# Performance work log

Measured on AMD Instinct MI355X. Metric: run time of the kernel, lower is better.

The kernel has to match this reference:

```python
import jax, jax.numpy as jnp
import numpy as np

EPS = 1e-6
NEG_SLOPE = 0.01  # torch LeakyReLU default

def ln(x, g, b):
    m = jnp.mean(x, axis=-1, keepdims=True)
    v = jnp.mean((x - m) ** 2, axis=-1, keepdims=True)
    return (x - m) / jnp.sqrt(v + EPS) * g + b

def leaky(x):
    return jnp.where(x >= 0, x, NEG_SLOPE * x)

def setup_inputs() -> dict:
    B, L, F, H, NH, LBL = 8, 1024, 1024, 256, 8, 4766
    key = jax.random.key(0)
    ks = jax.random.split(key, 16)
    def lin(k, i, o, s=0.03):
        kw, kb = jax.random.split(k)
        return jax.random.normal(kw, (i, o), jnp.float32) * s, jnp.zeros((o,), jnp.float32)
    w_in, b_in = lin(ks[0], F, H)
    w_h, b_h = lin(ks[1], H, H)
    a_w1, a_b1 = lin(ks[2], H, 64)
    a_w2, a_b2 = lin(ks[3], 64, NH)
    o_w1, o_b1 = lin(ks[4], NH * H, NH * H)
    o_w2, o_b2 = lin(ks[5], NH * H, LBL)
    CM = (jax.random.uniform(ks[6], (LBL, LBL)) < 0.002).astype(jnp.float32)
    CM = jnp.maximum(CM, jnp.eye(LBL, dtype=jnp.float32))
    return {
        'h_V': jax.random.normal(ks[7], (B, L, F), jnp.float32),
        'mask': jnp.ones((B, L), jnp.int32),
        'ln0_g': jnp.ones((F,), jnp.float32), 'ln0_b': jnp.zeros((F,), jnp.float32),
        'w_in': w_in, 'b_in': b_in,
        'ln1_g': jnp.ones((H,), jnp.float32), 'ln1_b': jnp.zeros((H,), jnp.float32),
        'w_h': w_h, 'b_h': b_h,
        'ln2_g': jnp.ones((H,), jnp.float32), 'ln2_b': jnp.zeros((H,), jnp.float32),
        'a_w1': a_w1, 'a_b1': a_b1,
        'a_lng': jnp.ones((64,), jnp.float32), 'a_lnb': jnp.zeros((64,), jnp.float32),
        'a_w2': a_w2, 'a_b2': a_b2,
        'o_w1': o_w1, 'o_b1': o_b1,
        'o_lng': jnp.ones((NH * H,), jnp.float32), 'o_lnb': jnp.zeros((NH * H,), jnp.float32),
        'o_w2': o_w2, 'o_b2': o_b2,
        'CM': CM,
    }

def reference(h_V, mask, ln0_g, ln0_b, w_in, b_in, ln1_g, ln1_b, w_h, b_h,
              ln2_g, ln2_b, a_w1, a_b1, a_lng, a_lnb, a_w2, a_b2,
              o_w1, o_b1, o_lng, o_lnb, o_w2, o_b2, CM):
    B = h_V.shape[0]
    # input + hidden blocks (eval mode: dropout is identity)
    x = ln(h_V, ln0_g, ln0_b)
    x = leaky(x @ w_in + b_in)
    x = ln(x, ln1_g, ln1_b)
    x = leaky(x @ w_h + b_h)
    x = ln(x, ln2_g, ln2_b)                      # [B,L,H]
    # multi-head attention pooling over sequence
    a = leaky(x @ a_w1 + a_b1)
    a = ln(a, a_lng, a_lnb)
    a = a @ a_w2 + a_b2                          # [B,L,NH]
    a = jnp.where(mask[:, :, None] == 0, jnp.float32(-1e9), a)
    a = jax.nn.softmax(a, axis=1)
    h = jnp.einsum('blh,bld->bhd', a, x).reshape(B, -1)  # [B,NH*H]
    # output block
    h = leaky(h @ o_w1 + o_b1)
    h = ln(h, o_lng, o_lnb)
    p = jax.nn.sigmoid(h @ o_w2 + o_b2)          # [B,LBL]
    # GO-hierarchy max-product propagation (eval path)
    out = jnp.max(p[:, None, :] * CM[None, :, :], axis=-1)  # [B,LBL]
    return out.astype(jnp.float32)
```

## Files before the change

### kernel.cpp

```cpp
#include <hip/hip_runtime.h>
#include <hip/hip_bf16.h>
#include <cstdint>

#define B_   8
#define L_   1024
#define F_   1024
#define H_   256
#define NH_  8
#define LBL_ 4766
#define M_   (B_*L_)
#define OD_  (NH_*H_)
#define NCM  (LBL_*LBL_)
#define MP_EPB 16384
#define MP_NB  ((NCM + MP_EPB - 1) / MP_EPB)

typedef unsigned short u16;
typedef unsigned int   u32;
typedef __attribute__((ext_vector_type(8))) short short8;
typedef __attribute__((ext_vector_type(4))) float float4v;

#define BF16_ONES_PAIR 0x3f803f80u

__device__ __forceinline__ float bf2f(u32 u) { return __uint_as_float(u << 16); }
__device__ __forceinline__ u16 f2bf(float f) {
    u32 u = __float_as_uint(f);
    u32 r = 0x7fffu + ((u >> 16) & 1u);
    return (u16)((u + r) >> 16);
}

struct f8 { float v[8]; };

__device__ __forceinline__ float ldS(const void* p, size_t i, bool bf) {
    return bf ? bf2f(((const u16*)p)[i]) : ((const float*)p)[i];
}
__device__ __forceinline__ float4 ld4(const void* p, size_t i, bool bf) {
    if (bf) {
        uint2 u = *(const uint2*)((const u16*)p + i);
        return make_float4(bf2f(u.x & 0xffff), bf2f(u.x >> 16),
                           bf2f(u.y & 0xffff), bf2f(u.y >> 16));
    }
    return *(const float4*)((const float*)p + i);
}
__device__ __forceinline__ f8 ld8(const void* p, size_t i, bool bf) {
    f8 r;
    if (bf) {
        uint4 u = *(const uint4*)((const u16*)p + i);
        r.v[0]=bf2f(u.x&0xffff); r.v[1]=bf2f(u.x>>16);
        r.v[2]=bf2f(u.y&0xffff); r.v[3]=bf2f(u.y>>16);
        r.v[4]=bf2f(u.z&0xffff); r.v[5]=bf2f(u.z>>16);
        r.v[6]=bf2f(u.w&0xffff); r.v[7]=bf2f(u.w>>16);
    } else {
        const float* q = (const float*)p + i;
        float4 a = *(const float4*)q, b = *(const float4*)(q+4);
        r.v[0]=a.x; r.v[1]=a.y; r.v[2]=a.z; r.v[3]=a.w;
        r.v[4]=b.x; r.v[5]=b.y; r.v[6]=b.z; r.v[7]=b.w;
    }
    return r;
}

__device__ __forceinline__ float wave_sum(float v) {
    #pragma unroll
    for (int m = 1; m < 64; m <<= 1) v += __shfl_xor(v, m, 64);
    return v;
}
__device__ __forceinline__ float wave_max(float v) {
    #pragma unroll
    for (int m = 1; m < 64; m <<= 1) v = fmaxf(v, __shfl_xor(v, m, 64));
    return v;
}
__device__ __forceinline__ float blk_sum(float v, float* sh) {
    v = wave_sum(v);
    int w = threadIdx.x >> 6, nw = blockDim.x >> 6;
    if ((threadIdx.x & 63) == 0) sh[w] = v;
    __syncthreads();
    float s = sh[0];
    for (int i = 1; i < nw; ++i) s += sh[i];
    __syncthreads();
    return s;
}
__device__ __forceinline__ float blk_max(float v, float* sh) {
    v = wave_max(v);
    int w = threadIdx.x >> 6, nw = blockDim.x >> 6;
    if ((threadIdx.x & 63) == 0) sh[w] = v;
    __syncthreads();
    float s = sh[0];
    for (int i = 1; i < nw; ++i) s = fmaxf(s, sh[i]);
    __syncthreads();
    return s;
}

__global__ __launch_bounds__(256) void prep_k(const void* __restrict__ hv,
        const void* __restrict__ g0, const void* __restrict__ b0, u16* __restrict__ x0,
        const void* __restrict__ w_in, u16* __restrict__ wt1,
        const void* __restrict__ w_h,  u16* __restrict__ wt2,
        const void* __restrict__ aw1,  u16* __restrict__ wt3,
        float* __restrict__ zA, float* __restrict__ zB,
        const u32* __restrict__ probe) {
    __shared__ u16 tile[64][65];
    bool bf = (probe[0] == BF16_ONES_PAIR);
    int blk = blockIdx.x, t = threadIdx.x;
    if (blk < M_/4) {
        int row = (blk << 2) + (t >> 6);
        int l = t & 63;
        size_t base = (size_t)row * F_;
        float4 vv[4];
        float s = 0.f, q = 0.f;
        #pragma unroll
        for (int j = 0; j < 4; ++j) {
            float4 v = ld4(hv, base + l * 4 + j * 256, bf);
            vv[j] = v;
            s += v.x + v.y + v.z + v.w;
            q += v.x*v.x + v.y*v.y + v.z*v.z + v.w*v.w;
        }
        s = wave_sum(s);
        q = wave_sum(q);
        float mean = s * (1.f / F_);
        float rstd = rsqrtf(q * (1.f / F_) - mean * mean + 1e-6f);
        #pragma unroll
        for (int j = 0; j < 4; ++j) {
            int off = l * 4 + j * 256;
            float4 gg = ld4(g0, off, bf);
            float4 bb = ld4(b0, off, bf);
            float4 v = vv[j];
            u32 o0 = f2bf((v.x - mean) * rstd * gg.x + bb.x)
                   | ((u32)f2bf((v.y - mean) * rstd * gg.y + bb.y) << 16);
            u32 o1 = f2bf((v.z - mean) * rstd * gg.z + bb.z)
                   | ((u32)f2bf((v.w - mean) * rstd * gg.w + bb.w) << 16);
            *(uint2*)(x0 + base + off) = make_uint2(o0, o1);
        }
        return;
    }
    blk -= M_/4;
    const void* W = nullptr; u16* WT = nullptr; int K = 0, N = 0, kt = 0, nt = 0;
    if (blk < 64)      { W = w_in; WT = wt1; K = F_; N = H_; kt = blk & 15; nt = blk >> 4; }
    else if (blk < 80) { int j = blk - 64; W = w_h; WT = wt2; K = H_; N = H_; kt = j & 3; nt = j >> 2; }
    else if (blk < 84) { int j = blk - 80; W = aw1; WT = wt3; K = H_; N = 64; kt = j; nt = 0; }
    else {
        int j = blk - 84;
        if (j < 16) {
            float4* p = (float4*)zA;
            for (int i = j * 256 + t; i < 8192; i += 4096) p[i] = make_float4(0,0,0,0);
        } else {
            j -= 16;
            float4* p = (float4*)zB;
            for (int i = j * 256 + t; i < 13628; i += 4096) p[i] = make_float4(0,0,0,0);
        }
        return;
    }
    int kt0 = kt * 64, nt0 = nt * 64;
    int r = t >> 2, cq = (t & 3) * 16;
    #pragma unroll
    for (int j = 0; j < 4; ++j) {
        float4 v = ld4(W, (size_t)(kt0 + r) * N + nt0 + cq + j * 4, bf);
        tile[r][cq + j*4 + 0] = f2bf(v.x);
        tile[r][cq + j*4 + 1] = f2bf(v.y);
        tile[r][cq + j*4 + 2] = f2bf(v.z);
        tile[r][cq + j*4 + 3] = f2bf(v.w);
    }
    __syncthreads();
    #pragma unroll
    for (int j = 0; j < 4; ++j) {
        int k = cq + j * 4;
        u32 a0 = tile[k+0][r], a1 = tile[k+1][r], a2 = tile[k+2][r], a3 = tile[k+3][r];
        uint2 o; o.x = a0 | (a1 << 16); o.y = a2 | (a3 << 16);
        *(uint2*)(WT + (size_t)(nt0 + r) * K + kt0 + k) = o;
    }
}

__global__ __launch_bounds__(256) void gemm_mfma(const u16* __restrict__ Ap, int amode,
        const float2* __restrict__ statin, const void* __restrict__ g,
        const void* __restrict__ bta, const u16* __restrict__ WT,
        const void* __restrict__ bias, u16* __restrict__ C,
        float* __restrict__ statout, int M, int N, int K,
        const u32* __restrict__ probe) {
    __shared__ short8 As[2][64][5];
    __shared__ short8 Bs[2][64][5];
    bool pbf = (probe[0] == BF16_ONES_PAIR);
    int t = threadIdx.x;
    int m0 = blockIdx.x * 64, n0 = blockIdx.y * 64;
    int r = t >> 2, kq = t & 3;
    int l = t & 63, w = t >> 6;
    int q = l >> 4, ml = l & 15;
    float4v acc[4];
    #pragma unroll
    for (int nt = 0; nt < 4; ++nt)
        #pragma unroll
        for (int i = 0; i < 4; ++i) acc[nt][i] = 0.f;
    float stm = 0.f, str = 1.f;
    if (amode == 1) {
        float2 st = statin[m0 + r];
        float mm = st.x * (1.f / K);
        stm = mm;
        str = rsqrtf(st.y * (1.f / K) - mm * mm + 1e-6f);
    }
    const size_t arow = (size_t)(m0 + r) * K;
    const size_t brow = (size_t)(n0 + r) * K;
    auto loadA = [&](int kk) -> short8 {
        if (amode == 1) {
            f8 a  = ld8(Ap, arow + kk, true);
            f8 gg = ld8(g, kk, pbf);
            f8 bb = ld8(bta, kk, pbf);
            short8 pa;
            #pragma unroll
            for (int j = 0; j < 8; ++j)
                pa[j] = (short)f2bf((a.v[j] - stm) * str * gg.v[j] + bb.v[j]);
            return pa;
        }
        return *(const short8*)(Ap + arow + kk);
    };
    {
        short8 pa = loadA(kq * 8);
        short8 pb = *(const short8*)(WT + brow + kq * 8);
        As[0][r][kq] = pa;
        Bs[0][r][kq] = pb;
    }
    __syncthreads();
    int nIt = K >> 5, cur = 0;
    for (int it = 0; it < nIt; ++it) {
        bool more = (it + 1 < nIt);
        short8 na, nb;
        if (more) {
            int kk = (it + 1) * 32 + kq * 8;
            na = loadA(kk);
            nb = *(const short8*)(WT + brow + kk);
        }
        short8 af = As[cur][w * 16 + ml][q];
        #pragma unroll
        for (int nt = 0; nt < 4; ++nt)
            acc[nt] = __builtin_amdgcn_mfma_f32_16x16x32_bf16(af, Bs[cur][nt*16 + ml][q],
                                                              acc[nt], 0, 0, 0);
        if (more) {
            As[cur ^ 1][r][kq] = na;
            Bs[cur ^ 1][r][kq] = nb;
            __syncthreads();
            cur ^= 1;
        }
    }
    float ov[4][4];
    #pragma unroll
    for (int nt = 0; nt < 4; ++nt) {
        int nn = n0 + nt * 16 + ml;
        float bv = ldS(bias, nn, pbf);
        #pragma unroll
        for (int reg = 0; reg < 4; ++reg) {
            float v = acc[nt][reg] + bv;
            v = v >= 0.f ? v : 0.01f * v;
            ov[nt][reg] = v;
            C[(size_t)(m0 + w * 16 + q * 4 + reg) * N + nn] = f2bf(v);
        }
    }
    if (statout) {
        #pragma unroll
        for (int reg = 0; reg < 4; ++reg) {
            float sv = ov[0][reg] + ov[1][reg] + ov[2][reg] + ov[3][reg];
            float qv = ov[0][reg]*ov[0][reg] + ov[1][reg]*ov[1][reg]
                     + ov[2][reg]*ov[2][reg] + ov[3][reg]*ov[3][reg];
            #pragma unroll
            for (int mk = 1; mk < 16; mk <<= 1) {
                sv += __shfl_xor(sv, mk, 64);
                qv += __shfl_xor(qv, mk, 64);
            }
            if (ml == 0) {
                int row = m0 + w * 16 + q * 4 + reg;
                atomicAdd(&statout[2 * row],     sv);
                atomicAdd(&statout[2 * row + 1], qv);
            }
        }
    }
}

__global__ __launch_bounds__(256) void gemm3_attn_k(const u16* __restrict__ Ap,
        const float2* __restrict__ statin, const void* __restrict__ g,
        const void* __restrict__ bta, const u16* __restrict__ WT,
        const void* __restrict__ bias,
        const void* __restrict__ alng, const void* __restrict__ alnb,
        const void* __restrict__ aw2, const void* __restrict__ ab2,
        const int* __restrict__ mask, float* __restrict__ lg,
        const u32* __restrict__ probe) {
    __shared__ short8 As[2][64][5];
    __shared__ short8 Bs[2][64][5];
    __shared__ float at[64][65];
    __shared__ float w2s[512];
    __shared__ float b2s[8];
    __shared__ float gs[64], bs[64];
    bool pbf = (probe[0] == BF16_ONES_PAIR);
    const int K = 256;
    int t = threadIdx.x;
    int m0 = blockIdx.x * 64;
    int r = t >> 2, kq = t & 3;
    int l = t & 63, w = t >> 6;
    int q = l >> 4, ml = l & 15;
    float4v acc[4];
    #pragma unroll
    for (int nt = 0; nt < 4; ++nt)
        #pragma unroll
        for (int i = 0; i < 4; ++i) acc[nt][i] = 0.f;
    float2 st = statin[m0 + r];
    float stm = st.x * (1.f / K);
    float str = rsqrtf(st.y * (1.f / K) - stm * stm + 1e-6f);
    const size_t arow = (size_t)(m0 + r) * K;
    const size_t brow = (size_t)r * K;
    auto loadA = [&](int kk) -> short8 {
        f8 a  = ld8(Ap, arow + kk, true);
        f8 gg = ld8(g, kk, pbf);
        f8 bb = ld8(bta, kk, pbf);
        short8 pa;
        #pragma unroll
        for (int j = 0; j < 8; ++j)
            pa[j] = (short)f2bf((a.v[j] - stm) * str * gg.v[j] + bb.v[j]);
        return pa;
    };
    {
        short8 pa = loadA(kq * 8);
        short8 pb = *(const short8*)(WT + brow + kq * 8);
        As[0][r][kq] = pa;
        Bs[0][r][kq] = pb;
    }
    __syncthreads();
    int cur = 0;
    #pragma unroll
    for (int it = 0; it < 8; ++it) {
        bool more = (it < 7);
        short8 na, nb;
        if (more) {
            int kk = (it + 1) * 32 + kq * 8;
            na = loadA(kk);
            nb = *(const short8*)(WT + brow + kk);
        }
        short8 af = As[cur][w * 16 + ml][q];
        #pragma unroll
        for (int nt = 0; nt < 4; ++nt)
            acc[nt] = __builtin_amdgcn_mfma_f32_16x16x32_bf16(af, Bs[cur][nt*16 + ml][q],
                                                              acc[nt], 0, 0, 0);
        if (more) {
            As[cur ^ 1][r][kq] = na;
            Bs[cur ^ 1][r][kq] = nb;
            __syncthreads();
            cur ^= 1;
        }
    }
    for (int i = t; i < 512; i += 256) w2s[i] = ldS(aw2, i, pbf);
    if (t < 8) b2s[t] = ldS(ab2, t, pbf);
    if (t < 64) { gs[t] = ldS(alng, t, pbf); bs[t] = ldS(alnb, t, pbf); }
    #pragma unroll
    for (int nt = 0; nt < 4; ++nt) {
        int nn = nt * 16 + ml;
        float bv = ldS(bias, nn, pbf);
        #pragma unroll
        for (int reg = 0; reg < 4; ++reg) {
            float v = acc[nt][reg] + bv;
            v = v >= 0.f ? v : 0.01f * v;
            at[w * 16 + q * 4 + reg][nn] = v;
        }
    }
    __syncthreads();
    int row = t >> 2, s4 = t & 3;
    float av[16];
    float sum = 0.f, sq = 0.f;
    #pragma unroll
    for (int j = 0; j < 16; ++j) {
        float v = at[row][s4 * 16 + j];
        av[j] = v; sum += v; sq += v * v;
    }
    sum += __shfl_xor(sum, 1, 64); sum += __shfl_xor(sum, 2, 64);
    sq  += __shfl_xor(sq, 1, 64);  sq  += __shfl_xor(sq, 2, 64);
    float mr = sum * (1.f / 64);
    float rr = rsqrtf(sq * (1.f / 64) - mr * mr + 1e-6f);
    float val[16];
    #pragma unroll
    for (int j = 0; j < 16; ++j)
        val[j] = (av[j] - mr) * rr * gs[s4 * 16 + j] + bs[s4 * 16 + j];
    float hv[8];
    #pragma unroll
    for (int h = 0; h < 8; ++h) {
        float p = 0.f;
        #pragma unroll
        for (int j = 0; j < 16; ++j) p += val[j] * w2s[(s4 * 16 + j) * 8 + h];
        p += __shfl_xor(p, 1, 64);
        p += __shfl_xor(p, 2, 64);
        hv[h] = p + b2s[h];
    }
    if (s4 == 0) {
        int gr = m0 + row;
        bool mz = (mask[gr] == 0);
        int bb_ = gr >> 10, ll = gr & 1023;
        #pragma unroll
        for (int h = 0; h < 8; ++h) {
            float v = mz ? -1e9f : hv[h];
            lg[((size_t)bb_ * NH_ + h) * L_ + ll] = v;
        }
    }
}

__global__ __launch_bounds__(1024) void attnpool_k(const float* __restrict__ lg,
        const float2* __restrict__ st2, const u16* __restrict__ x2,
        const void* __restrict__ g, const void* __restrict__ b,
        float* __restrict__ hp, const u32* __restrict__ probe) {
    __shared__ float aw_s[1024];
    __shared__ float part[16][256];
    __shared__ float sh[16];
    bool pbf = (probe[0] == BF16_ONES_PAIR);
    int bh = blockIdx.x, t = threadIdx.x;
    int bb = bh >> 3;
    float v = lg[(size_t)bh * L_ + t];
    float mx = blk_max(v, sh);
    float e = expf(v - mx);
    float s = blk_sum(e, sh);
    float inv = 1.f / s;
    float2 st = st2[(bb << 10) + t];
    float m = st.x * (1.f / 256);
    float r = rsqrtf(st.y * (1.f / 256) - m * m + 1e-6f);
    float aw = e * inv * r;
    aw_s[t] = aw;
    float c1 = blk_sum(aw * m, sh);
    int chunk = t >> 6, d0 = (t & 63) * 4;
    const u16* xb = x2 + ((size_t)(bb << 10) + chunk * 64) * 256;
    const float* awc = aw_s + chunk * 64;
    float a0 = 0.f, a1 = 0.f, a2 = 0.f, a3 = 0.f;
    #pragma unroll 8
    for (int i = 0; i < 64; ++i) {
        uint2 u = *(const uint2*)(xb + (size_t)i * 256 + d0);
        float wv = awc[i];
        a0 += wv * bf2f(u.x & 0xffff);
        a1 += wv * bf2f(u.x >> 16);
        a2 += wv * bf2f(u.y & 0xffff);
        a3 += wv * bf2f(u.y >> 16);
    }
    *(float4*)&part[chunk][d0] = make_float4(a0, a1, a2, a3);
    __syncthreads();
    if (t < 256) {
        float S = 0.f;
        #pragma unroll
        for (int c = 0; c < 16; ++c) S += part[c][t];
        hp[(size_t)bh * 256 + t] = (S - c1) * ldS(g, t, pbf) + ldS(b, t, pbf);
    }
}

template<int KC>
__global__ __launch_bounds__(256) void gemv_ilp_k(const float* __restrict__ hv,
        const void* __restrict__ W, float* __restrict__ acc, int K, int N,
        const u32* __restrict__ probe) {
    __shared__ float hs[8 * KC];
    bool bf = (probe[0] == BF16_ONES_PAIR);
    int t = threadIdx.x;
    int kb = blockIdx.y * KC;
    for (int i = t; i < 8 * KC; i += 256) {
        int r = i / KC, k = i & (KC - 1);
        hs[i] = hv[(size_t)r * K + kb + k];
    }
    __syncthreads();
    int c0 = (blockIdx.x * 256 + t) * 2;
    if (c0 >= N) return;
    float a[8][2] = {};
    if (bf) {
        const u16* Wp = (const u16*)W;
        #pragma unroll
        for (int h = 0; h < KC / 32; ++h) {
            u32 wr[32];
            #pragma unroll
            for (int i = 0; i < 32; ++i)
                wr[i] = *(const u32*)(Wp + (size_t)(kb + h * 32 + i) * N + c0);
            #pragma unroll
            for (int i = 0; i < 32; ++i) {
                float w0 = bf2f(wr[i] & 0xffff), w1 = bf2f(wr[i] >> 16);
                #pragma unroll
                for (int r = 0; r < 8; ++r) {
                    float hh = hs[r * KC + h * 32 + i];
                    a[r][0] += hh * w0; a[r][1] += hh * w1;
                }
            }
        }
    } else {
        const float* Wp = (const float*)W;
        #pragma unroll
        for (int h = 0; h < KC / 16; ++h) {
            float2 wr[16];
            #pragma unroll
            for (int i = 0; i < 16; ++i)
                wr[i] = *(const float2*)(Wp + (size_t)(kb + h * 16 + i) * N + c0);
            #pragma unroll
            for (int i = 0; i < 16; ++i) {
                #pragma unroll
                for (int r = 0; r < 8; ++r) {
                    float hh = hs[r * KC + h * 16 + i];
                    a[r][0] += hh * wr[i].x; a[r][1] += hh * wr[i].y;
                }
            }
        }
    }
    bool ok1 = (c0 + 1 < N);
    #pragma unroll
    for (int r = 0; r < 8; ++r) {
        atomicAdd(&acc[(size_t)r * N + c0], a[r][0]);
        if (ok1) atomicAdd(&acc[(size_t)r * N + c0 + 1], a[r][1]);
    }
}

__global__ __launch_bounds__(256) void out_ln_k(float* __restrict__ h,
        const void* __restrict__ bias, const void* __restrict__ g,
        const void* __restrict__ b, const u32* __restrict__ probe) {
    __shared__ float sh[4];
    bool bf = (probe[0] == BF16_ONES_PAIR);
    int row = blockIdx.x, t = threadIdx.x;
    float v[8];
    float s = 0.f, q = 0.f;
    #pragma unroll
    for (int i = 0; i < 8; ++i) {
        int c = t + i * 256;
        float x = h[(size_t)row * OD_ + c] + ldS(bias, c, bf);
        x = x >= 0.f ? x : 0.01f * x;
        v[i] = x; s += x; q += x * x;
    }
    s = blk_sum(s, sh) * (1.f / OD_);
    q = blk_sum(q, sh) * (1.f / OD_);
    float rstd = rsqrtf(q - s * s + 1e-6f);
    #pragma unroll
    for (int i = 0; i < 8; ++i) {
        int c = t + i * 256;
        h[(size_t)row * OD_ + c] = (v[i] - s) * rstd * ldS(g, c, bf) + ldS(b, c, bf);
    }
}

__global__ __launch_bounds__(256) void sigmoid_t_k(const float* __restrict__ acc,
        const void* __restrict__ bias, float* __restrict__ pt,
        float* __restrict__ out, const u32* __restrict__ probe) {
    bool bf = (probe[0] == BF16_ONES_PAIR);
    int c = blockIdx.x * 256 + threadIdx.x;
    if (c >= LBL_) return;
    float bv = ldS(bias, c, bf);
    float o[8];
    #pragma unroll
    for (int r = 0; r < 8; ++r) {
        float v = acc[(size_t)r * LBL_ + c] + bv;
        o[r] = 1.f / (1.f + expf(-v));
        out[(size_t)r * LBL_ + c] = 0.f;
    }
    float4* dst = (float4*)(pt + (size_t)c * 8);
    dst[0] = make_float4(o[0], o[1], o[2], o[3]);
    dst[1] = make_float4(o[4], o[5], o[6], o[7]);
}

__device__ __forceinline__ void mp_hit(u32 idx, float cmv,
        const float* __restrict__ pt, int* smax, u32 rowBase) {
    u32 i = idx / LBL_;
    u32 j = idx - i * LBL_;
    const float4* pj = (const float4*)(pt + (size_t)j * 8);
    float4 pa = pj[0], pb = pj[1];
    int base = (int)(i - rowBase) * 8;
    atomicMax(&smax[base + 0], __float_as_int(pa.x * cmv));
    atomicMax(&smax[base + 1], __float_as_int(pa.y * cmv));
    atomicMax(&smax[base + 2], __float_as_int(pa.z * cmv));
    atomicMax(&smax[base + 3], __float_as_int(pa.w * cmv));
    atomicMax(&smax[base + 4], __float_as_int(pb.x * cmv));
    atomicMax(&smax[base + 5], __float_as_int(pb.y * cmv));
    atomicMax(&smax[base + 6], __float_as_int(pb.z * cmv));
    atomicMax(&smax[base + 7], __float_as_int(pb.w * cmv));
}

__global__ __launch_bounds__(256) void maxprod3_k(const float* __restrict__ pt,
        const void* __restrict__ CM, float* __restrict__ out,
        const u32* __restrict__ probe) {
    __shared__ int smax[6 * 8];
    bool bf = (probe[0] == BF16_ONES_PAIR);
    int t = threadIdx.x;
    size_t blockStart = (size_t)blockIdx.x * MP_EPB;
    u32 rowBase = (u32)(blockStart / LBL_);
    for (int i = t; i < 48; i += 256) smax[i] = 0;
    __syncthreads();
    if (bf) {
        const u16* cm = (const u16*)CM;
        uint4 ch[8];
        size_t i0[8];
        #pragma unroll
        for (int u = 0; u < 8; ++u) {
            size_t idx0 = blockStart + ((size_t)u * 256 + t) * 8;
            i0[u] = idx0;
            ch[u] = (idx0 + 8 <= NCM) ? *(const uint4*)(cm + idx0)
                                      : make_uint4(0, 0, 0, 0);
        }
        #pragma unroll
        for (int u = 0; u < 8; ++u) {
            size_t idx0 = i0[u];
            if (idx0 + 8 <= NCM) {
                uint4 c4 = ch[u];
                if ((c4.x | c4.y | c4.z | c4.w) == 0) continue;
                u32 hw[4] = {c4.x, c4.y, c4.z, c4.w};
                #pragma unroll
                for (int d = 0; d < 4; ++d) {
                    u32 lo = hw[d] & 0xffff, hi = hw[d] >> 16;
                    if (lo) mp_hit((u32)idx0 + d*2,     bf2f(lo), pt, smax, rowBase);
                    if (hi) mp_hit((u32)idx0 + d*2 + 1, bf2f(hi), pt, smax, rowBase);
                }
            } else if (idx0 < NCM) {
                for (u32 e = 0; e < (u32)(NCM - idx0); ++e) {
                    u16 h = cm[idx0 + e];
                    if (h) mp_hit((u32)idx0 + e, bf2f(h), pt, smax, rowBase);
                }
            }
        }
    } else {
        const float* cm = (const float*)CM;
        #pragma unroll
        for (int u = 0; u < 16; ++u) {
            size_t idx0 = blockStart + ((size_t)u * 256 + t) * 4;
            if (idx0 >= NCM) continue;
            float v[4];
            if (idx0 + 4 <= NCM) {
                float4 f = *(const float4*)(cm + idx0);
                v[0] = f.x; v[1] = f.y; v[2] = f.z; v[3] = f.w;
            } else {
                v[0] = v[1] = v[2] = v[3] = 0.f;
                for (u32 e = 0; e < (u32)(NCM - idx0); ++e) v[e] = cm[idx0 + e];
            }
            if (v[0] == 0.f && v[1] == 0.f && v[2] == 0.f && v[3] == 0.f) continue;
            #pragma unroll
            for (int e = 0; e < 4; ++e)
                if (v[e] != 0.f) mp_hit((u32)idx0 + e, v[e], pt, smax, rowBase);
        }
    }
    __syncthreads();
    size_t lastIdx = blockStart + MP_EPB - 1;
    if (lastIdx >= NCM) lastIdx = NCM - 1;
    int nrows = (int)((u32)(lastIdx / LBL_) - rowBase) + 1;
    for (int s = t; s < nrows * 8; s += 256) {
        int v = smax[s];
        if (v != 0) {
            int rr = s >> 3, b = s & 7;
            atomicMax((int*)(out + (size_t)b * LBL_ + rowBase + rr), v);
        }
    }
}

extern "C" void kernel_launch(void* const* d_in, const int* in_sizes, int n_in,
                              void* d_out, int out_size, void* d_ws, size_t ws_size,
                              hipStream_t stream) {
    const void* hv   = d_in[0];
    const int* mask  = (const int*)d_in[1];
    const void* ln0g = d_in[2];
    const void* ln0b = d_in[3];
    const void* w_in = d_in[4];
    const void* b_in = d_in[5];
    const void* ln1g = d_in[6];
    const void* ln1b = d_in[7];
    const void* w_h  = d_in[8];
    const void* b_h  = d_in[9];
    const void* ln2g = d_in[10];
    const void* ln2b = d_in[11];
    const void* aw1  = d_in[12];
    const void* ab1  = d_in[13];
    const void* alng = d_in[14];
    const void* alnb = d_in[15];
    const void* aw2  = d_in[16];
    const void* ab2  = d_in[17];
    const void* ow1  = d_in[18];
    const void* ob1  = d_in[19];
    const void* olng = d_in[20];
    const void* olnb = d_in[21];
    const void* ow2  = d_in[22];
    const void* ob2  = d_in[23];
    const void* CM   = d_in[24];
    const u32* probe = (const u32*)ln0g;
    float* out = (float*)d_out;

    float* f = (float*)d_ws;
    float2* st1 = (float2*)f;
    float2* st2 = st1 + 8192;
    float* lg = f + 32768;
    float* c1 = lg + 65536;
    float* Sp = c1 + 64;
    float* hp = Sp + 131072;
    float* ha = hp + 16384;
    float* l2 = ha + 16384;
    float* pt = l2 + 38128;
    u16* x0  = (u16*)(pt + 38128);
    u16* x1  = x0 + 8388608;
    u16* x2  = x1 + 2097152;
    u16* abr = x2 + 2097152;
    u16* wt1 = abr + 524288;
    u16* wt2 = wt1 + 262144;
    u16* wt3 = wt2 + 65536;

    prep_k<<<M_/4 + 84 + 32, 256, 0, stream>>>(hv, ln0g, ln0b, x0,
                                               w_in, wt1, w_h, wt2, aw1, wt3,
                                               f, ha, probe);
    gemm_mfma<<<dim3(M_/64, 4), 256, 0, stream>>>(x0, 2, nullptr, nullptr, nullptr,
                                                  wt1, b_in, x1, (float*)st1,
                                                  M_, H_, F_, probe);
    gemm_mfma<<<dim3(M_/64, 4), 256, 0, stream>>>(x1, 1, st1, ln1g, ln1b,
                                                  wt2, b_h, x2, (float*)st2,
                                                  M_, H_, H_, probe);
    gemm3_attn_k<<<M_/64, 256, 0, stream>>>(x2, st2, ln2g, ln2b, wt3, ab1,
                                            alng, alnb, aw2, ab2, mask, lg, probe);
    attnpool_k<<<B_*NH_, 1024, 0, stream>>>(lg, st2, x2, ln2g, ln2b, hp, probe);
    gemv_ilp_k<32><<<dim3(OD_/512, OD_/32), 256, 0, stream>>>(hp, ow1, ha, OD_, OD_, probe);
    out_ln_k<<<B_, 256, 0, stream>>>(ha, ob1, olng, olnb, probe);
    gemv_ilp_k<64><<<dim3((LBL_+511)/512, OD_/64), 256, 0, stream>>>(ha, ow2, l2, OD_, LBL_, probe);
    sigmoid_t_k<<<(LBL_+255)/256, 256, 0, stream>>>(l2, ob2, pt, out, probe);
    maxprod3_k<<<MP_NB, 256, 0, stream>>>(pt, CM, out, probe);
}
```

Baseline: 343.8 us.

## Replace atomic split-K GEMV with partial-sum buffers reduced in consumer kernels

Both output-block GEMVs now write per-K-chunk partial results to workspace buffers (16 chunks of 128) instead of accumulating with atomicAdd. The reductions move into out_ln_k and sigmoid_t_k, and prep_k no longer zeroes the second accumulator. Each thread now handles one column, reads the weights as scalars and takes the hidden vector straight from global memory instead of staging it in LDS. This removes atomic contention and some zeroing, but drops the two-column vectorised weight loads and adds partial-buffer traffic, while cutting the K-split count from 64 or 32 blocks per column down to 16.

New measurement: 371.8 us. 8.2% more time.

```diff
diff --git a/kernel.cpp b/kernel.cpp
--- a/kernel.cpp
+++ b/kernel.cpp
@@ -13,6 +13,7 @@
 #define NCM  (LBL_*LBL_)
 #define MP_EPB 16384
 #define MP_NB  ((NCM + MP_EPB - 1) / MP_EPB)
+#define NKC  16
 
 typedef unsigned short u16;
 typedef unsigned int   u32;
@@ -94,7 +95,7 @@
         const void* __restrict__ w_in, u16* __restrict__ wt1,
         const void* __restrict__ w_h,  u16* __restrict__ wt2,
         const void* __restrict__ aw1,  u16* __restrict__ wt3,
-        float* __restrict__ zA, float* __restrict__ zB,
+        float* __restrict__ zA,
         const u32* __restrict__ probe) {
     __shared__ u16 tile[64][65];
     bool bf = (probe[0] == BF16_ONES_PAIR);
@@ -137,14 +138,8 @@
     else if (blk < 84) { int j = blk - 80; W = aw1; WT = wt3; K = H_; N = 64; kt = j; nt = 0; }
     else {
         int j = blk - 84;
-        if (j < 16) {
-            float4* p = (float4*)zA;
-            for (int i = j * 256 + t; i < 8192; i += 4096) p[i] = make_float4(0,0,0,0);
-        } else {
-            j -= 16;
-            float4* p = (float4*)zB;
-            for (int i = j * 256 + t; i < 13628; i += 4096) p[i] = make_float4(0,0,0,0);
-        }
+        float4* p = (float4*)zA;
+        for (int i = j * 256 + t; i < 8192; i += 4096) p[i] = make_float4(0,0,0,0);
         return;
     }
     int kt0 = kt * 64, nt0 = nt * 64;
@@ -437,68 +432,57 @@
 }
 
 template<int KC>
-__global__ __launch_bounds__(256) void gemv_ilp_k(const float* __restrict__ hv,
-        const void* __restrict__ W, float* __restrict__ acc, int K, int N,
+__global__ __launch_bounds__(256) void gemv_part_k(const float* __restrict__ hvec,
+        const void* __restrict__ W, float* __restrict__ part, int K, int N,
         const u32* __restrict__ probe) {
-    __shared__ float hs[8 * KC];
     bool bf = (probe[0] == BF16_ONES_PAIR);
     int t = threadIdx.x;
+    int c = blockIdx.x * 256 + t;
     int kb = blockIdx.y * KC;
-    for (int i = t; i < 8 * KC; i += 256) {
-        int r = i / KC, k = i & (KC - 1);
-        hs[i] = hv[(size_t)r * K + kb + k];
-    }
-    __syncthreads();
-    int c0 = (blockIdx.x * 256 + t) * 2;
-    if (c0 >= N) return;
-    float a[8][2] = {};
+    if (c >= N) return;
+    float a[8] = {0.f,0.f,0.f,0.f,0.f,0.f,0.f,0.f};
+    const float* hb = hvec + kb;
     if (bf) {
-        const u16* Wp = (const u16*)W;
-        #pragma unroll
-        for (int h = 0; h < KC / 32; ++h) {
-            u32 wr[32];
-            #pragma unroll
-            for (int i = 0; i < 32; ++i)
-                wr[i] = *(const u32*)(Wp + (size_t)(kb + h * 32 + i) * N + c0);
-            #pragma unroll
-            for (int i = 0; i < 32; ++i) {
-                float w0 = bf2f(wr[i] & 0xffff), w1 = bf2f(wr[i] >> 16);
-                #pragma unroll
-                for (int r = 0; r < 8; ++r) {
-                    float hh = hs[r * KC + h * 32 + i];
-                    a[r][0] += hh * w0; a[r][1] += hh * w1;
-                }
-            }
-        }
-    } else {
-        const float* Wp = (const float*)W;
-        #pragma unroll
-        for (int h = 0; h < KC / 16; ++h) {
-            float2 wr[16];
+        const u16* Wp = (const u16*)W + (size_t)kb * N + c;
+        #pragma unroll
+        for (int kk = 0; kk < KC; kk += 16) {
+            float w[16];
             #pragma unroll
             for (int i = 0; i < 16; ++i)
-                wr[i] = *(const float2*)(Wp + (size_t)(kb + h * 16 + i) * N + c0);
+                w[i] = bf2f(Wp[(size_t)(kk + i) * N]);
             #pragma unroll
             for (int i = 0; i < 16; ++i) {
                 #pragma unroll
-                for (int r = 0; r < 8; ++r) {
-                    float hh = hs[r * KC + h * 16 + i];
-                    a[r][0] += hh * wr[i].x; a[r][1] += hh * wr[i].y;
-                }
+                for (int r = 0; r < 8; ++r)
+                    a[r] += hb[r * K + kk + i] * w[i];
             }
         }
-    }
-    bool ok1 = (c0 + 1 < N);
-    #pragma unroll
-    for (int r = 0; r < 8; ++r) {
-        atomicAdd(&acc[(size_t)r * N + c0], a[r][0]);
-        if (ok1) atomicAdd(&acc[(size_t)r * N + c0 + 1], a[r][1]);
-    }
-}
-
-__global__ __launch_bounds__(256) void out_ln_k(float* __restrict__ h,
-        const void* __restrict__ bias, const void* __restrict__ g,
-        const void* __restrict__ b, const u32* __restrict__ probe) {
+    } else {
+        const float* Wp = (const float*)W + (size_t)kb * N + c;
+        #pragma unroll
+        for (int kk = 0; kk < KC; kk += 16) {
+            float w[16];
+            #pragma unroll
+            for (int i = 0; i < 16; ++i)
+                w[i] = Wp[(size_t)(kk + i) * N];
+            #pragma unroll
+            for (int i = 0; i < 16; ++i) {
+                #pragma unroll
+                for (int r = 0; r < 8; ++r)
+                    a[r] += hb[r * K + kk + i] * w[i];
+            }
+        }
+    }
+    float* dst = part + ((size_t)blockIdx.y * 8) * N + c;
+    #pragma unroll
+    for (int r = 0; r < 8; ++r)
+        dst[(size_t)r * N] = a[r];
+}
+
+__global__ __launch_bounds__(256) void out_ln_k(const float* __restrict__ part,
+        float* __restrict__ h, const void* __restrict__ bias,
+        const void* __restrict__ g, const void* __restrict__ b,
+        const u32* __restrict__ probe) {
     __shared__ float sh[4];
     bool bf = (probe[0] == BF16_ONES_PAIR);
     int row = blockIdx.x, t = threadIdx.x;
@@ -507,7 +491,10 @@
     #pragma unroll
     for (int i = 0; i < 8; ++i) {
         int c = t + i * 256;
-        float x = h[(size_t)row * OD_ + c] + ldS(bias, c, bf);
+        float x = ldS(bias, c, bf);
+        #pragma unroll
+        for (int ch = 0; ch < NKC; ++ch)
+            x += part[((size_t)ch * 8 + row) * OD_ + c];
         x = x >= 0.f ? x : 0.01f * x;
         v[i] = x; s += x; q += x * x;
     }
@@ -521,7 +508,7 @@
     }
 }
 
-__global__ __launch_bounds__(256) void sigmoid_t_k(const float* __restrict__ acc,
+__global__ __launch_bounds__(256) void sigmoid_t_k(const float* __restrict__ part,
         const void* __restrict__ bias, float* __restrict__ pt,
         float* __restrict__ out, const u32* __restrict__ probe) {
     bool bf = (probe[0] == BF16_ONES_PAIR);
@@ -531,7 +518,10 @@
     float o[8];
     #pragma unroll
     for (int r = 0; r < 8; ++r) {
-        float v = acc[(size_t)r * LBL_ + c] + bv;
+        float v = bv;
+        #pragma unroll
+        for (int ch = 0; ch < NKC; ++ch)
+            v += part[((size_t)ch * 8 + r) * LBL_ + c];
         o[r] = 1.f / (1.f + expf(-v));
         out[(size_t)r * LBL_ + c] = 0.f;
     }
@@ -665,24 +655,22 @@
     float* f = (float*)d_ws;
     float2* st1 = (float2*)f;
     float2* st2 = st1 + 8192;
-    float* lg = f + 32768;
-    float* c1 = lg + 65536;
-    float* Sp = c1 + 64;
-    float* hp = Sp + 131072;
-    float* ha = hp + 16384;
-    float* l2 = ha + 16384;
-    float* pt = l2 + 38128;
+    float* lg    = f + 32768;
+    float* hp    = lg + 65536;
+    float* ha    = hp + 16384;
+    float* part1 = ha + 16384;
+    float* part2 = part1 + 262144;
+    float* pt    = part2 + 610048;
     u16* x0  = (u16*)(pt + 38128);
     u16* x1  = x0 + 8388608;
     u16* x2  = x1 + 2097152;
-    u16* abr = x2 + 2097152;
-    u16* wt1 = abr + 524288;
+    u16* wt1 = x2 + 2097152;
     u16* wt2 = wt1 + 262144;
     u16* wt3 = wt2 + 65536;
 
-    prep_k<<<M_/4 + 84 + 32, 256, 0, stream>>>(hv, ln0g, ln0b, x0,
+    prep_k<<<M_/4 + 84 + 16, 256, 0, stream>>>(hv, ln0g, ln0b, x0,
                                                w_in, wt1, w_h, wt2, aw1, wt3,
-                                               f, ha, probe);
+                                               f, probe);
     gemm_mfma<<<dim3(M_/64, 4), 256, 0, stream>>>(x0, 2, nullptr, nullptr, nullptr,
                                                   wt1, b_in, x1, (float*)st1,
                                                   M_, H_, F_, probe);
@@ -692,9 +680,11 @@
     gemm3_attn_k<<<M_/64, 256, 0, stream>>>(x2, st2, ln2g, ln2b, wt3, ab1,
                                             alng, alnb, aw2, ab2, mask, lg, probe);
     attnpool_k<<<B_*NH_, 1024, 0, stream>>>(lg, st2, x2, ln2g, ln2b, hp, probe);
-    gemv_ilp_k<32><<<dim3(OD_/512, OD_/32), 256, 0, stream>>>(hp, ow1, ha, OD_, OD_, probe);
-    out_ln_k<<<B_, 256, 0, stream>>>(ha, ob1, olng, olnb, probe);
-    gemv_ilp_k<64><<<dim3((LBL_+511)/512, OD_/64), 256, 0, stream>>>(ha, ow2, l2, OD_, LBL_, probe);
-    sigmoid_t_k<<<(LBL_+255)/256, 256, 0, stream>>>(l2, ob2, pt, out, probe);
+    gemv_part_k<128><<<dim3(OD_/256, NKC), 256, 0, stream>>>(hp, ow1, part1,
+                                                             OD_, OD_, probe);
+    out_ln_k<<<B_, 256, 0, stream>>>(part1, ha, ob1, olng, olnb, probe);
+    gemv_part_k<128><<<dim3((LBL_+255)/256, NKC), 256, 0, stream>>>(ha, ow2, part2,
+                                                                    OD_, LBL_, probe);
+    sigmoid_t_k<<<(LBL_+255)/256, 256, 0, stream>>>(part2, ob2, pt, out, probe);
     maxprod3_k<<<MP_NB, 256, 0, stream>>>(pt, CM, out, probe);
 }
```
